# Kernel optimization log

Measured on AMD Instinct MI355X. Metric: run time of the kernel, lower is better.

## Reference

```python
import jax, jax.numpy as jnp
import numpy as np

NUM_ITER = 2
NUM_BINS = 10
BIN_DISP = 0.5
MIN_FILTER_REG = 1e-05
STEPLEN_REG = 0.0


def distance_map(center, sz, num_bins, bin_disp):
    # center: (2,) float; sz: (sz0, sz1). Returns (num_bins, sz0, sz1).
    k0 = jnp.arange(sz[0], dtype=jnp.float32)
    k1 = jnp.arange(sz[1], dtype=jnp.float32)
    d0 = k0 - center[0]
    d1 = k1 - center[1]
    dist = jnp.sqrt(d0[:, None] ** 2 + d1[None, :] ** 2)
    bc = jnp.arange(num_bins, dtype=jnp.float32)
    bin_diff = dist[None] / bin_disp - bc[:, None, None]
    rest = jax.nn.relu(1.0 - jnp.abs(bin_diff[:-1]))
    last = jnp.clip(1.0 + bin_diff[-1:], 0.0, 1.0)
    return jnp.concatenate([rest, last], axis=0)


def unfold_map(full_map, H, W):
    # full_map: (2H-1, 2W-1). Emulates F.unfold(...,(H,W)).view(H,W,H,W).flip((2,3)).permute(2,3,0,1)
    # result m[py, px, ky, kx] = full_map[(H-1)-py+ky, (W-1)-px+kx]
    py = jnp.arange(H); ky = jnp.arange(H)
    px = jnp.arange(W); kx = jnp.arange(W)
    iy = (H - 1) - py[:, None] + ky[None, :]          # (H, H) [py, ky]
    ix = (W - 1) - px[:, None] + kx[None, :]          # (W, W) [px, kx]
    m = full_map[iy[:, None, :, None], ix[None, :, None, :]]  # (H, W, H, W)
    return m.reshape(1, 1, H * W, H, W)


def setup_inputs() -> dict:
    key = jax.random.key(0)
    k1, k2, k3 = jax.random.split(key, 3)
    B, NF, C, H, W = 2, 4096, 256, 64, 64
    filter_map = jax.random.normal(k1, (B, NF, C, 1, 1), jnp.float32) / 16.0
    reference_feat = jax.random.normal(k2, (1, B, C, H, W), jnp.float32)
    query_feat = jax.random.normal(k3, (1, B, C, H, W), jnp.float32)
    # learned 1x1-conv predictor weights, initialized exactly as in __init__
    d = jnp.arange(NUM_BINS, dtype=jnp.float32) * BIN_DISP
    init_gauss = jnp.exp(-0.5 * (d / 1.0) ** 2)          # init_gauss_sigma = 1.0
    w_label = init_gauss - init_gauss.min()
    w_spatial = jnp.ones((NUM_BINS,), jnp.float32)
    w_mask = 4.0 * jnp.tanh(2.0 - d)                     # v_minus_init_factor = 4.0, sigmoid act
    log_step_length = jnp.zeros((1,), jnp.float32)       # log(1.0)
    filter_reg = 0.01 * jnp.ones((1,), jnp.float32)
    return {"filter_map": filter_map, "reference_feat": reference_feat,
            "query_feat": query_feat, "w_label": w_label, "w_spatial": w_spatial,
            "w_mask": w_mask, "log_step_length": log_step_length, "filter_reg": filter_reg}


def reference(filter_map, reference_feat, query_feat, w_label, w_spatial, w_mask,
              log_step_length, filter_reg):
    B, NF, C = filter_map.shape[:3]
    H, W = reference_feat.shape[-2], reference_feat.shape[-1]
    filt = filter_map.reshape(B, NF, C)
    feat = reference_feat[0]                              # (B, C, H, W)

    dist_sz = (2 * H - 1, 2 * W - 1)
    center = jnp.array([dist_sz[0] // 2, dist_sz[1] // 2], jnp.float32)
    dmap = distance_map(center, dist_sz, NUM_BINS, BIN_DISP)   # (K, 2H-1, 2W-1)
    label_full = jnp.einsum('k,kyx->yx', w_label, dmap)
    vplus_full = jnp.einsum('k,kyx->yx', w_spatial, dmap)
    wm_full = jax.nn.sigmoid(jnp.einsum('k,kyx->yx', w_mask, dmap))
    target_map = unfold_map(label_full, H, W)             # (1,1,NF,H,W)
    v_plus = unfold_map(vplus_full, H, W)
    weight_m = unfold_map(wm_full, H, W)

    sl = jnp.exp(log_step_length)[0]
    rw = jnp.maximum(filter_reg[0] * filter_reg[0], MIN_FILTER_REG ** 2)

    a = weight_m
    for _ in range(NUM_ITER):
        # apply_filter: 1x1 filters as grouped conv == batched matmul
        scores = jnp.einsum('bcyx,bfc->bfyx', feat, filt)[None]        # (1,B,NF,H,W)
        # LeakyReluPar and its derivative, weighted by v_plus
        act = v_plus * (0.5 * (1.0 - a) * jnp.abs(scores) + 0.5 * (1.0 + a) * scores)
        dact = v_plus * (0.5 * (1.0 - a) * jnp.sign(scores) + 0.5 * (1.0 + a))
        res = act - v_plus * target_map
        mres = dact * res
        # apply_feat_transpose with 1x1 filter size
        fgrad_loss = jnp.einsum('bfyx,bcyx->bfc', mres[0], feat)
        fgrad = rw * filt + fgrad_loss
        # step length alpha (steepest descent / Gauss-Newton step)
        sg = jnp.einsum('bcyx,bfc->bfyx', feat, fgrad)[None]
        den_res = dact * sg
        alpha_den = jnp.sum((den_res * den_res).reshape(B, NF, -1), axis=2)
        alpha_num = jnp.sum((fgrad * fgrad).reshape(B, NF, -1), axis=2)
        alpha_den = jnp.maximum(alpha_den + (rw + STEPLEN_REG) * alpha_num, 1e-8)
        alpha = alpha_num / alpha_den                                   # (B, NF)
        filt = filt - (sl * alpha)[:, :, None] * fgrad
    return filt.reshape(B, NF, C, 1, 1)
```

## Files before the change

kernel.cpp:

```cpp
#include <hip/hip_runtime.h>


#define NFILT 4096
#define CDIM  256
#define HWDIM 4096

typedef _Float16 f16;
typedef _Float16 f16x8 __attribute__((ext_vector_type(8)));
typedef _Float16 f16x4 __attribute__((ext_vector_type(4)));
typedef float f32x4 __attribute__((ext_vector_type(4)));

#define MFMA(a, b, c) __builtin_amdgcn_mfma_f32_16x16x32_f16((a), (b), (c), 0, 0, 0)

#define STAGE(g, gstride, col0, lds, R)                                         \
  {                                                                             \
    _Pragma("unroll")                                                           \
    for (int i_ = 0; i_ < (R) / 32; ++i_) {                                     \
      const int rbase_ = w * ((R) / 4) + i_ * 8;                                \
      const int row_   = rbase_ + (lane >> 3);                                  \
      const int slot_  = lane & 7;                                              \
      const int col_   = (col0) + ((slot_ ^ (row_ & 7)) << 3);                  \
      __builtin_amdgcn_global_load_lds(                                         \
          (const __attribute__((address_space(1))) void*)                       \
              ((g) + (size_t)row_ * (gstride) + col_),                          \
          (__attribute__((address_space(3))) void*)((lds) + rbase_ * 64),       \
          16, 0, 0);                                                            \
    }                                                                           \
  }

#define LIDX(row, slot) (((row) * 64) + ((((slot) ^ ((row) & 7))) << 3))

__global__ __launch_bounds__(256) void k_maps(
    const float* __restrict__ wl, const float* __restrict__ wsp,
    const float* __restrict__ wmk, float4* __restrict__ tbl)
{
  int i = blockIdx.x * 256 + threadIdx.x;
  if (i >= 127 * 127) return;
  int yy = i / 127, xx = i - yy * 127;
  float dy = (float)yy - 63.f, dx = (float)xx - 63.f;
  float d2 = 2.f * sqrtf(dy * dy + dx * dx);
  float l = 0.f, v = 0.f, m = 0.f;
#pragma unroll
  for (int k = 0; k < 9; ++k) {
    float t = fmaxf(1.f - fabsf(d2 - (float)k), 0.f);
    l += wl[k] * t; v += wsp[k] * t; m += wmk[k] * t;
  }
  float t9 = fminf(fmaxf(d2 - 8.f, 0.f), 1.f);
  l += wl[9] * t9; v += wsp[9] * t9; m += wmk[9] * t9;
  tbl[i] = make_float4(v * l, v, 1.f / (1.f + expf(-m)), 0.f);
}

__global__ __launch_bounds__(256) void k_convert(
    const float* __restrict__ feat, f16* __restrict__ featc,
    f16* __restrict__ featT)
{
  __shared__ float tbuf[64][65];
  int bid = blockIdx.x;
  int b = bid >> 8, cb = (bid >> 6) & 3, yb = bid & 63;
  int ty = threadIdx.x & 63, tc = threadIdx.x >> 6;
  const float* src = feat + ((size_t)b * CDIM + cb * 64) * HWDIM + yb * 64;
#pragma unroll
  for (int s = 0; s < 16; ++s) {
    int c = s * 4 + tc;
    float v = src[(size_t)c * HWDIM + ty];
    tbuf[c][ty] = v;
    featc[((size_t)b * CDIM + cb * 64 + c) * HWDIM + yb * 64 + ty] = (f16)v;
  }
  __syncthreads();
#pragma unroll
  for (int s = 0; s < 16; ++s) {
    int y = s * 4 + tc;
    featT[((size_t)b * HWDIM + yb * 64 + y) * CDIM + cb * 64 + ty] = (f16)tbuf[ty][y];
  }
}

__global__ __launch_bounds__(256) void k_filt16(
    const float* __restrict__ src, float* __restrict__ dst32,
    f16* __restrict__ dst16)
{
  const int i = blockIdx.x * 256 + threadIdx.x;
  const float4 v = ((const float4*)src)[i];
  ((float4*)dst32)[i] = v;
  f16x4 h; h[0] = (f16)v.x; h[1] = (f16)v.y; h[2] = (f16)v.z; h[3] = (f16)v.w;
  *(f16x4*)&dst16[(size_t)i * 4] = h;
}

__global__ __launch_bounds__(256) void k_score(
    const f16* __restrict__ filt16, const f16* __restrict__ featT,
    const float4* __restrict__ tbl, f16* __restrict__ mres,
    unsigned long long* __restrict__ sgn)
{
  __shared__ f16 As0[128 * 64], As1[128 * 64], Bs0[128 * 64], Bs1[128 * 64];
  const int tid = threadIdx.x, w = tid >> 6, lane = tid & 63;
  const int llo = lane & 15, lhi = lane >> 4;
  const int wr = w >> 1, wc = w & 1;
  const int b = blockIdx.z;
  const int fb = blockIdx.x * 128, yxb = blockIdx.y * 128;
  const f16* A  = filt16 + ((size_t)b * NFILT + fb) * CDIM;
  const f16* Bg = featT  + ((size_t)b * HWDIM + yxb) * CDIM;

  f32x4 acc[4][4] = {};
  STAGE(A,  CDIM, 0, As0, 128);
  STAGE(Bg, CDIM, 0, Bs0, 128);
  __syncthreads();

  auto kstep = [&](const f16* Ac, const f16* Bc, f16* An, f16* Bn, int coln) {
    f16x8 av[4], bv[4];
#pragma unroll
    for (int mi = 0; mi < 4; ++mi)
      av[mi] = *(const f16x8*)&Ac[LIDX(wr * 64 + mi * 16 + llo, lhi)];
#pragma unroll
    for (int ni = 0; ni < 4; ++ni)
      bv[ni] = *(const f16x8*)&Bc[LIDX(wc * 64 + ni * 16 + llo, lhi)];
    if (An) { STAGE(A, CDIM, coln, An, 128); STAGE(Bg, CDIM, coln, Bn, 128); }
#pragma unroll
    for (int mi = 0; mi < 4; ++mi)
#pragma unroll
      for (int ni = 0; ni < 4; ++ni)
        acc[mi][ni] = MFMA(av[mi], bv[ni], acc[mi][ni]);
#pragma unroll
    for (int mi = 0; mi < 4; ++mi)
      av[mi] = *(const f16x8*)&Ac[LIDX(wr * 64 + mi * 16 + llo, 4 + lhi)];
#pragma unroll
    for (int ni = 0; ni < 4; ++ni)
      bv[ni] = *(const f16x8*)&Bc[LIDX(wc * 64 + ni * 16 + llo, 4 + lhi)];
#pragma unroll
    for (int mi = 0; mi < 4; ++mi)
#pragma unroll
      for (int ni = 0; ni < 4; ++ni)
        acc[mi][ni] = MFMA(av[mi], bv[ni], acc[mi][ni]);
    __syncthreads();
  };
  kstep(As0, Bs0, As1, Bs1, 64);
  kstep(As1, Bs1, As0, Bs0, 128);
  kstep(As0, Bs0, As1, Bs1, 192);
  kstep(As1, Bs1, (f16*)nullptr, (f16*)nullptr, 0);

  unsigned long long sbits = 0ull;
#pragma unroll
  for (int mi = 0; mi < 4; ++mi)
#pragma unroll
    for (int ni = 0; ni < 4; ++ni)
#pragma unroll
      for (int r = 0; r < 4; ++r) {
        const int f  = fb + wr * 64 + mi * 16 + lhi * 4 + r;
        const int yx = yxb + wc * 64 + ni * 16 + llo;
        const int y = yx >> 6, x = yx & 63;
        const int t = (63 - (f >> 6) + y) * 127 + (63 - (f & 63) + x);
        const float4 tv = tbl[t];
        const float s  = acc[mi][ni][r];
        const float q  = 0.5f * tv.y;
        const float qa = q * tv.z;
        const float h1 = q - qa, h2 = q + qa;
        const float sg0 = (s > 0.f) ? 1.f : ((s < 0.f) ? -1.f : 0.f);
        const float act = h1 * fabsf(s) + h2 * s;
        const float dct = h1 * sg0 + h2;
        mres[((size_t)b * NFILT + f) * HWDIM + yx] = (f16)(dct * (act - tv.x));
        sbits |= (unsigned long long)(s > 0.f ? 1 : 0) << ((mi * 4 + ni) * 4 + r);
      }
  sgn[(((size_t)b * 32 + blockIdx.x) * 32 + blockIdx.y) * 256 + tid] = sbits;
}

__global__ __launch_bounds__(256) void k_floss(
    const f16* __restrict__ mres, const f16* __restrict__ featc,
    f16* __restrict__ fpart)
{
  __shared__ f16 As0[64 * 64], As1[64 * 64], Bs0[128 * 64], Bs1[128 * 64];
  const int tid = threadIdx.x, w = tid >> 6, lane = tid & 63;
  const int llo = lane & 15, lhi = lane >> 4;
  const int bz = blockIdx.z, b = bz >> 2, s = bz & 3;
  const int fbl = blockIdx.x * 64, cb = blockIdx.y * 128;
  const int k0 = s * 1024;
  const f16* A  = mres  + ((size_t)b * NFILT + fbl) * HWDIM;
  const f16* Bg = featc + ((size_t)b * CDIM + cb) * HWDIM;

  f32x4 acc[4][2] = {};
  STAGE(A,  HWDIM, k0, As0, 64);
  STAGE(Bg, HWDIM, k0, Bs0, 128);
  __syncthreads();

  auto kstep = [&](const f16* Ac, const f16* Bc, f16* An, f16* Bn, int coln) {
    f16x8 av[4], bv[2];
#pragma unroll
    for (int mi = 0; mi < 4; ++mi)
      av[mi] = *(const f16x8*)&Ac[LIDX(mi * 16 + llo, lhi)];
#pragma unroll
    for (int ni = 0; ni < 2; ++ni)
      bv[ni] = *(const f16x8*)&Bc[LIDX(w * 32 + ni * 16 + llo, lhi)];
    if (An) { STAGE(A, HWDIM, coln, An, 64); STAGE(Bg, HWDIM, coln, Bn, 128); }
#pragma unroll
    for (int mi = 0; mi < 4; ++mi)
#pragma unroll
      for (int ni = 0; ni < 2; ++ni)
        acc[mi][ni] = MFMA(av[mi], bv[ni], acc[mi][ni]);
#pragma unroll
    for (int mi = 0; mi < 4; ++mi)
      av[mi] = *(const f16x8*)&Ac[LIDX(mi * 16 + llo, 4 + lhi)];
#pragma unroll
    for (int ni = 0; ni < 2; ++ni)
      bv[ni] = *(const f16x8*)&Bc[LIDX(w * 32 + ni * 16 + llo, 4 + lhi)];
#pragma unroll
    for (int mi = 0; mi < 4; ++mi)
#pragma unroll
      for (int ni = 0; ni < 2; ++ni)
        acc[mi][ni] = MFMA(av[mi], bv[ni], acc[mi][ni]);
    __syncthreads();
  };
#pragma unroll
  for (int ks = 0; ks < 16; ++ks) {
    const bool odd = ks & 1;
    kstep(odd ? As1 : As0, odd ? Bs1 : Bs0,
          ks < 15 ? (odd ? As0 : As1) : (f16*)nullptr,
          ks < 15 ? (odd ? Bs0 : Bs1) : (f16*)nullptr,
          k0 + (ks + 1) * 64);
  }

#pragma unroll
  for (int mi = 0; mi < 4; ++mi)
#pragma unroll
    for (int ni = 0; ni < 2; ++ni)
#pragma unroll
      for (int r = 0; r < 4; ++r) {
        const int f = fbl + mi * 16 + lhi * 4 + r;
        const int c = cb + w * 32 + ni * 16 + llo;
        fpart[(((size_t)b * 4 + s) * NFILT + f) * CDIM + c] = (f16)acc[mi][ni][r];
      }
}

__global__ __launch_bounds__(256) void k_fgrad(
    const f16* __restrict__ fpart, const float* __restrict__ filt32,
    const float* __restrict__ freg,
    float* __restrict__ fgrad32, f16* __restrict__ fgrad16,
    float* __restrict__ anum)
{
  const int tid = threadIdx.x, w = tid >> 6, lane = tid & 63;
  const int f = blockIdx.x * 4 + w, b = blockIdx.y;
  const float fr = freg[0];
  const float rw = fmaxf(fr * fr, 1e-10f);
  float4 sum = make_float4(0.f, 0.f, 0.f, 0.f);
#pragma unroll
  for (int s = 0; s < 4; ++s) {
    f16x4 p = *(const f16x4*)&fpart[(((size_t)b * 4 + s) * NFILT + f) * CDIM + lane * 4];
    sum.x += (float)p[0]; sum.y += (float)p[1];
    sum.z += (float)p[2]; sum.w += (float)p[3];
  }
  const size_t row4 = ((size_t)b * NFILT + f) * 64 + lane;
  const float4 fv = ((const float4*)filt32)[row4];
  float4 fg;
  fg.x = rw * fv.x + sum.x; fg.y = rw * fv.y + sum.y;
  fg.z = rw * fv.z + sum.z; fg.w = rw * fv.w + sum.w;
  ((float4*)fgrad32)[row4] = fg;
  f16x4 h; h[0] = (f16)fg.x; h[1] = (f16)fg.y; h[2] = (f16)fg.z; h[3] = (f16)fg.w;
  *(f16x4*)&fgrad16[row4 * 4] = h;
  float ss = fg.x * fg.x + fg.y * fg.y + fg.z * fg.z + fg.w * fg.w;
  ss += __shfl_xor(ss, 1);  ss += __shfl_xor(ss, 2);  ss += __shfl_xor(ss, 4);
  ss += __shfl_xor(ss, 8);  ss += __shfl_xor(ss, 16); ss += __shfl_xor(ss, 32);
  if (lane == 0) anum[b * NFILT + f] = ss;
}

__global__ __launch_bounds__(256) void k_sg(
    const f16* __restrict__ fgrad16, const f16* __restrict__ featT,
    const float4* __restrict__ tbl, const unsigned long long* __restrict__ sgn,
    float* __restrict__ denp)
{
  __shared__ f16 As0[128 * 64], As1[128 * 64], Bs0[128 * 64], Bs1[128 * 64];
  const int tid = threadIdx.x, w = tid >> 6, lane = tid & 63;
  const int llo = lane & 15, lhi = lane >> 4;
  const int wr = w >> 1, wc = w & 1;
  const int b = blockIdx.z;
  const int fb = blockIdx.x * 128, yxb = blockIdx.y * 128;
  const f16* A  = fgrad16 + ((size_t)b * NFILT + fb) * CDIM;
  const f16* Bg = featT   + ((size_t)b * HWDIM + yxb) * CDIM;

  f32x4 acc[4][4] = {};
  STAGE(A,  CDIM, 0, As0, 128);
  STAGE(Bg, CDIM, 0, Bs0, 128);
  __syncthreads();

  auto kstep = [&](const f16* Ac, const f16* Bc, f16* An, f16* Bn, int coln) {
    f16x8 av[4], bv[4];
#pragma unroll
    for (int mi = 0; mi < 4; ++mi)
      av[mi] = *(const f16x8*)&Ac[LIDX(wr * 64 + mi * 16 + llo, lhi)];
#pragma unroll
    for (int ni = 0; ni < 4; ++ni)
      bv[ni] = *(const f16x8*)&Bc[LIDX(wc * 64 + ni * 16 + llo, lhi)];
    if (An) { STAGE(A, CDIM, coln, An, 128); STAGE(Bg, CDIM, coln, Bn, 128); }
#pragma unroll
    for (int mi = 0; mi < 4; ++mi)
#pragma unroll
      for (int ni = 0; ni < 4; ++ni)
        acc[mi][ni] = MFMA(av[mi], bv[ni], acc[mi][ni]);
#pragma unroll
    for (int mi = 0; mi < 4; ++mi)
      av[mi] = *(const f16x8*)&Ac[LIDX(wr * 64 + mi * 16 + llo, 4 + lhi)];
#pragma unroll
    for (int ni = 0; ni < 4; ++ni)
      bv[ni] = *(const f16x8*)&Bc[LIDX(wc * 64 + ni * 16 + llo, 4 + lhi)];
#pragma unroll
    for (int mi = 0; mi < 4; ++mi)
#pragma unroll
      for (int ni = 0; ni < 4; ++ni)
        acc[mi][ni] = MFMA(av[mi], bv[ni], acc[mi][ni]);
    __syncthreads();
  };
  kstep(As0, Bs0, As1, Bs1, 64);
  kstep(As1, Bs1, As0, Bs0, 128);
  kstep(As0, Bs0, As1, Bs1, 192);
  kstep(As1, Bs1, (f16*)nullptr, (f16*)nullptr, 0);

  const unsigned long long sbits =
      sgn[(((size_t)b * 32 + blockIdx.x) * 32 + blockIdx.y) * 256 + tid];
  float dacc[4][4] = {};
#pragma unroll
  for (int mi = 0; mi < 4; ++mi)
#pragma unroll
    for (int ni = 0; ni < 4; ++ni)
#pragma unroll
      for (int r = 0; r < 4; ++r) {
        const int f  = fb + wr * 64 + mi * 16 + lhi * 4 + r;
        const int yx = yxb + wc * 64 + ni * 16 + llo;
        const int y = yx >> 6, x = yx & 63;
        const int t = (63 - (f >> 6) + y) * 127 + (63 - (f & 63) + x);
        const float4 tv = tbl[t];
        const float q  = 0.5f * tv.y;
        const float qa = q * tv.z;
        const float h1 = q - qa, h2 = q + qa;
        const float sg0 = ((sbits >> ((mi * 4 + ni) * 4 + r)) & 1ull) ? 1.f : -1.f;
        const float dct = h1 * sg0 + h2;
        const float dr  = dct * acc[mi][ni][r];
        dacc[mi][r] += dr * dr;
      }
#pragma unroll
  for (int mi = 0; mi < 4; ++mi)
#pragma unroll
    for (int r = 0; r < 4; ++r) {
      float v = dacc[mi][r];
      v += __shfl_xor(v, 1); v += __shfl_xor(v, 2);
      v += __shfl_xor(v, 4); v += __shfl_xor(v, 8);
      if (llo == 0)
        denp[((size_t)b * 64 + blockIdx.y * 2 + wc) * NFILT +
             fb + wr * 64 + mi * 16 + lhi * 4 + r] = v;
    }
}

__global__ __launch_bounds__(256) void k_update(
    float* __restrict__ filt32, const float* __restrict__ fgrad32,
    const float* __restrict__ anum, const float* __restrict__ denp,
    const float* __restrict__ lsl, const float* __restrict__ freg,
    f16* __restrict__ filt16o)
{
  const int i = blockIdx.x * 256 + threadIdx.x;
  const int bf = i >> 6, cq = i & 63;
  const int b = bf >> 12, f = bf & (NFILT - 1);
  const float fr = freg[0];
  const float rw = fmaxf(fr * fr, 1e-10f);
  const float sl = expf(lsl[0]);
  float den = 0.f;
#pragma unroll
  for (int j = 0; j < 64; ++j) den += denp[((size_t)b * 64 + j) * NFILT + f];
  const float num = anum[bf];
  const float alpha = num / fmaxf(den + rw * num, 1e-8f);
  const float st = sl * alpha;
  const size_t row4 = (size_t)bf * 64 + cq;
  const float4 fv = ((const float4*)filt32)[row4];
  const float4 gv = ((const float4*)fgrad32)[row4];
  float4 nv;
  nv.x = fv.x - st * gv.x; nv.y = fv.y - st * gv.y;
  nv.z = fv.z - st * gv.z; nv.w = fv.w - st * gv.w;
  ((float4*)filt32)[row4] = nv;
  f16x4 h; h[0] = (f16)nv.x; h[1] = (f16)nv.y; h[2] = (f16)nv.z; h[3] = (f16)nv.w;
  *(f16x4*)&filt16o[row4 * 4] = h;
}

extern "C" void kernel_launch(void* const* d_in, const int* in_sizes, int n_in,
                              void* d_out, int out_size, void* d_ws, size_t ws_size,
                              hipStream_t stream) {
  (void)in_sizes; (void)n_in; (void)out_size; (void)ws_size;
  const float* filt  = (const float*)d_in[0];
  const float* rfeat = (const float*)d_in[1];
  const float* wl  = (const float*)d_in[3];
  const float* wsp = (const float*)d_in[4];
  const float* wmk = (const float*)d_in[5];
  const float* lsl = (const float*)d_in[6];
  const float* fre = (const float*)d_in[7];

  char* ws = (char*)d_ws;
  float4* tbl    = (float4*)(ws + 0);
  f16* featc     = (f16*)(ws + 262144);
  f16* featT     = (f16*)(ws + 4456448);
  f16* filt16    = (f16*)(ws + 8650752);
  f16* fgrad16   = (f16*)(ws + 12845056);
  float* fgrad32 = (float*)(ws + 17039360);
  float* anum    = (float*)(ws + 25427968);
  float* denp    = (float*)(ws + 25460736);
  unsigned long long* sgn = (unsigned long long*)(ws + 27557888);
  f16* mres      = (f16*)(ws + 31752192);
  f16* fpart     = (f16*)(ws + 98861056);
  float* filt32  = (float*)d_out;

  k_maps<<<64, 256, 0, stream>>>(wl, wsp, wmk, tbl);
  k_convert<<<512, 256, 0, stream>>>(rfeat, featc, featT);
  k_filt16<<<2048, 256, 0, stream>>>(filt, filt32, filt16);

  for (int it = 0; it < 2; ++it) {
    k_score<<<dim3(32, 32, 2), 256, 0, stream>>>(filt16, featT, tbl, mres, sgn);
    k_floss<<<dim3(64, 2, 8), 256, 0, stream>>>(mres, featc, fpart);
    k_fgrad<<<dim3(1024, 2), 256, 0, stream>>>(fpart, filt32, fre,
                                               fgrad32, fgrad16, anum);
    k_sg<<<dim3(32, 32, 2), 256, 0, stream>>>(fgrad16, featT, tbl, sgn, denp);
    k_update<<<2048, 256, 0, stream>>>(filt32, fgrad32, anum, denp, lsl, fre,
                                       filt16);
  }
}
```

Baseline: 379.3 us.

## Enlarge floss tile, precompute leaky-relu slopes in table, shuffle-reduce denominator

The k_floss GEMM tile grows from 64x128 to 128x128 per block, with a 2x2 warp layout and 16 MFMAs per k-substep. This improves operand reuse and halves the number of blocks to 512. The distance-map table now stores the two leaky-relu slopes (v and v*sigmoid(m)), so the score and sg kernels simply select a slope by sign instead of recomputing h1/h2. k_update replaces its 64-load serial denominator sum per thread with one load per lane and a wavefront shuffle reduction. The risks are fewer blocks for the MI355X's CUs and more LDS and register pressure. The zero-score sign case also now uses the negative slope.

```diff
diff --git a/kernel.cpp b/kernel.cpp
--- a/kernel.cpp
+++ b/kernel.cpp
@@ -47,7 +47,8 @@
   }
   float t9 = fminf(fmaxf(d2 - 8.f, 0.f), 1.f);
   l += wl[9] * t9; v += wsp[9] * t9; m += wmk[9] * t9;
-  tbl[i] = make_float4(v * l, v, 1.f / (1.f + expf(-m)), 0.f);
+  const float wm = 1.f / (1.f + expf(-m));
+  tbl[i] = make_float4(v * l, v, v * wm, 0.f);
 }
 
 __global__ __launch_bounds__(256) void k_convert(
@@ -149,13 +150,9 @@
         const int t = (63 - (f >> 6) + y) * 127 + (63 - (f & 63) + x);
         const float4 tv = tbl[t];
         const float s  = acc[mi][ni][r];
-        const float q  = 0.5f * tv.y;
-        const float qa = q * tv.z;
-        const float h1 = q - qa, h2 = q + qa;
-        const float sg0 = (s > 0.f) ? 1.f : ((s < 0.f) ? -1.f : 0.f);
-        const float act = h1 * fabsf(s) + h2 * s;
-        const float dct = h1 * sg0 + h2;
-        mres[((size_t)b * NFILT + f) * HWDIM + yx] = (f16)(dct * (act - tv.x));
+        const float sel = (s > 0.f) ? tv.y : tv.z;
+        const float mr  = sel * fmaf(sel, s, -tv.x);
+        mres[((size_t)b * NFILT + f) * HWDIM + yx] = (f16)mr;
         sbits |= (unsigned long long)(s > 0.f ? 1 : 0) << ((mi * 4 + ni) * 4 + r);
       }
   sgn[(((size_t)b * 32 + blockIdx.x) * 32 + blockIdx.y) * 256 + tid] = sbits;
@@ -165,44 +162,45 @@
     const f16* __restrict__ mres, const f16* __restrict__ featc,
     f16* __restrict__ fpart)
 {
-  __shared__ f16 As0[64 * 64], As1[64 * 64], Bs0[128 * 64], Bs1[128 * 64];
+  __shared__ f16 As0[128 * 64], As1[128 * 64], Bs0[128 * 64], Bs1[128 * 64];
   const int tid = threadIdx.x, w = tid >> 6, lane = tid & 63;
   const int llo = lane & 15, lhi = lane >> 4;
+  const int wr = w >> 1, wc = w & 1;
   const int bz = blockIdx.z, b = bz >> 2, s = bz & 3;
-  const int fbl = blockIdx.x * 64, cb = blockIdx.y * 128;
+  const int fb = blockIdx.x * 128, cb = blockIdx.y * 128;
   const int k0 = s * 1024;
-  const f16* A  = mres  + ((size_t)b * NFILT + fbl) * HWDIM;
+  const f16* A  = mres  + ((size_t)b * NFILT + fb) * HWDIM;
   const f16* Bg = featc + ((size_t)b * CDIM + cb) * HWDIM;
 
-  f32x4 acc[4][2] = {};
-  STAGE(A,  HWDIM, k0, As0, 64);
+  f32x4 acc[4][4] = {};
+  STAGE(A,  HWDIM, k0, As0, 128);
   STAGE(Bg, HWDIM, k0, Bs0, 128);
   __syncthreads();
 
   auto kstep = [&](const f16* Ac, const f16* Bc, f16* An, f16* Bn, int coln) {
-    f16x8 av[4], bv[2];
-#pragma unroll
-    for (int mi = 0; mi < 4; ++mi)
-      av[mi] = *(const f16x8*)&Ac[LIDX(mi * 16 + llo, lhi)];
-#pragma unroll
-    for (int ni = 0; ni < 2; ++ni)
-      bv[ni] = *(const f16x8*)&Bc[LIDX(w * 32 + ni * 16 + llo, lhi)];
-    if (An) { STAGE(A, HWDIM, coln, An, 64); STAGE(Bg, HWDIM, coln, Bn, 128); }
-#pragma unroll
-    for (int mi = 0; mi < 4; ++mi)
-#pragma unroll
-      for (int ni = 0; ni < 2; ++ni)
-        acc[mi][ni] = MFMA(av[mi], bv[ni], acc[mi][ni]);
-#pragma unroll
-    for (int mi = 0; mi < 4; ++mi)
-      av[mi] = *(const f16x8*)&Ac[LIDX(mi * 16 + llo, 4 + lhi)];
-#pragma unroll
-    for (int ni = 0; ni < 2; ++ni)
-      bv[ni] = *(const f16x8*)&Bc[LIDX(w * 32 + ni * 16 + llo, 4 + lhi)];
-#pragma unroll
-    for (int mi = 0; mi < 4; ++mi)
-#pragma unroll
-      for (int ni = 0; ni < 2; ++ni)
+    f16x8 av[4], bv[4];
+#pragma unroll
+    for (int mi = 0; mi < 4; ++mi)
+      av[mi] = *(const f16x8*)&Ac[LIDX(wr * 64 + mi * 16 + llo, lhi)];
+#pragma unroll
+    for (int ni = 0; ni < 4; ++ni)
+      bv[ni] = *(const f16x8*)&Bc[LIDX(wc * 64 + ni * 16 + llo, lhi)];
+    if (An) { STAGE(A, HWDIM, coln, An, 128); STAGE(Bg, HWDIM, coln, Bn, 128); }
+#pragma unroll
+    for (int mi = 0; mi < 4; ++mi)
+#pragma unroll
+      for (int ni = 0; ni < 4; ++ni)
+        acc[mi][ni] = MFMA(av[mi], bv[ni], acc[mi][ni]);
+#pragma unroll
+    for (int mi = 0; mi < 4; ++mi)
+      av[mi] = *(const f16x8*)&Ac[LIDX(wr * 64 + mi * 16 + llo, 4 + lhi)];
+#pragma unroll
+    for (int ni = 0; ni < 4; ++ni)
+      bv[ni] = *(const f16x8*)&Bc[LIDX(wc * 64 + ni * 16 + llo, 4 + lhi)];
+#pragma unroll
+    for (int mi = 0; mi < 4; ++mi)
+#pragma unroll
+      for (int ni = 0; ni < 4; ++ni)
         acc[mi][ni] = MFMA(av[mi], bv[ni], acc[mi][ni]);
     __syncthreads();
   };
@@ -218,11 +216,11 @@
 #pragma unroll
   for (int mi = 0; mi < 4; ++mi)
 #pragma unroll
-    for (int ni = 0; ni < 2; ++ni)
+    for (int ni = 0; ni < 4; ++ni)
 #pragma unroll
       for (int r = 0; r < 4; ++r) {
-        const int f = fbl + mi * 16 + lhi * 4 + r;
-        const int c = cb + w * 32 + ni * 16 + llo;
+        const int f = fb + wr * 64 + mi * 16 + lhi * 4 + r;
+        const int c = cb + wc * 64 + ni * 16 + llo;
         fpart[(((size_t)b * 4 + s) * NFILT + f) * CDIM + c] = (f16)acc[mi][ni][r];
       }
 }
@@ -323,13 +321,9 @@
         const int y = yx >> 6, x = yx & 63;
         const int t = (63 - (f >> 6) + y) * 127 + (63 - (f & 63) + x);
         const float4 tv = tbl[t];
-        const float q  = 0.5f * tv.y;
-        const float qa = q * tv.z;
-        const float h1 = q - qa, h2 = q + qa;
-        const float sg0 = ((sbits >> ((mi * 4 + ni) * 4 + r)) & 1ull) ? 1.f : -1.f;
-        const float dct = h1 * sg0 + h2;
+        const float dct = ((sbits >> ((mi * 4 + ni) * 4 + r)) & 1ull) ? tv.y : tv.z;
         const float dr  = dct * acc[mi][ni][r];
-        dacc[mi][r] += dr * dr;
+        dacc[mi][r] = fmaf(dr, dr, dacc[mi][r]);
       }
 #pragma unroll
   for (int mi = 0; mi < 4; ++mi)
@@ -351,18 +345,19 @@
     f16* __restrict__ filt16o)
 {
   const int i = blockIdx.x * 256 + threadIdx.x;
-  const int bf = i >> 6, cq = i & 63;
+  const int bf = i >> 6, lane = threadIdx.x & 63;
   const int b = bf >> 12, f = bf & (NFILT - 1);
   const float fr = freg[0];
   const float rw = fmaxf(fr * fr, 1e-10f);
   const float sl = expf(lsl[0]);
-  float den = 0.f;
-#pragma unroll
-  for (int j = 0; j < 64; ++j) den += denp[((size_t)b * 64 + j) * NFILT + f];
+  float den = denp[((size_t)b * 64 + lane) * NFILT + f];
+  den += __shfl_xor(den, 1);  den += __shfl_xor(den, 2);
+  den += __shfl_xor(den, 4);  den += __shfl_xor(den, 8);
+  den += __shfl_xor(den, 16); den += __shfl_xor(den, 32);
   const float num = anum[bf];
   const float alpha = num / fmaxf(den + rw * num, 1e-8f);
   const float st = sl * alpha;
-  const size_t row4 = (size_t)bf * 64 + cq;
+  const size_t row4 = (size_t)bf * 64 + lane;
   const float4 fv = ((const float4*)filt32)[row4];
   const float4 gv = ((const float4*)fgrad32)[row4];
   float4 nv;
@@ -405,7 +400,7 @@
 
   for (int it = 0; it < 2; ++it) {
     k_score<<<dim3(32, 32, 2), 256, 0, stream>>>(filt16, featT, tbl, mres, sgn);
-    k_floss<<<dim3(64, 2, 8), 256, 0, stream>>>(mres, featc, fpart);
+    k_floss<<<dim3(32, 2, 8), 256, 0, stream>>>(mres, featc, fpart);
     k_fgrad<<<dim3(1024, 2), 256, 0, stream>>>(fpart, filt32, fre,
                                                fgrad32, fgrad16, anum);
     k_sg<<<dim3(32, 32, 2), 256, 0, stream>>>(fgrad16, featT, tbl, sgn, denp);
```

New measurement: 370.4 us. 1.02x faster.
